# Performance work log

Measured on AMD Instinct MI355X. Metric: run time of the kernel, lower is better.

## Reference

```python
import jax, jax.numpy as jnp
import numpy as np

B = 32768
T = 4096

def setup_inputs() -> dict:
    key = jax.random.key(0)
    k1, k2, k3 = jax.random.split(key, 3)
    q0 = jax.random.normal(k1, (B, 1), dtype=jnp.float32)
    # per-timestep Linear(1,1) weights/biases, flattened to [T]
    w = jax.random.normal(k2, (T,), dtype=jnp.float32)
    b = jax.random.normal(k3, (T,), dtype=jnp.float32)
    return {"q0": q0, "w": w, "b": b}

def reference(q0, w, b):
    # Original: u_seq[b, t, 0] = w[t] * q0[b, 0] + b[t]  (q never updates in the loop)
    # Single fused broadcast replaces T tiny GEMMs.
    u_seq = q0[:, None, :] * w[None, :, None] + b[None, :, None]  # [B, T, 1]
    return u_seq
```

## Files before the change

kernel.cpp:

```cpp
#include <hip/hip_runtime.h>
#include <hip/hip_bf16.h>


__global__ __launch_bounds__(256)
void pn_rowkernel(const float* __restrict__ q0,
                  const float4* __restrict__ w4,
                  const float4* __restrict__ b4,
                  float4* __restrict__ out4,
                  int T4) {
    const int row = blockIdx.x;
    const float q = q0[row];
    float4* __restrict__ orow = out4 + (long long)row * T4;
    for (int j = threadIdx.x; j < T4; j += blockDim.x) {
        const float4 wv = w4[j];
        const float4 bv = b4[j];
        float4 o;
        o.x = fmaf(q, wv.x, bv.x);
        o.y = fmaf(q, wv.y, bv.y);
        o.z = fmaf(q, wv.z, bv.z);
        o.w = fmaf(q, wv.w, bv.w);
        orow[j] = o;
    }
}

__global__ __launch_bounds__(256)
void pn_rowkernel_scalar(const float* __restrict__ q0,
                         const float* __restrict__ w,
                         const float* __restrict__ b,
                         float* __restrict__ out,
                         int T) {
    const int row = blockIdx.x;
    const float q = q0[row];
    float* __restrict__ orow = out + (long long)row * T;
    for (int j = threadIdx.x; j < T; j += blockDim.x) {
        orow[j] = fmaf(q, w[j], b[j]);
    }
}

extern "C" void kernel_launch(void* const* d_in, const int* in_sizes, int n_in,
                              void* d_out, int out_size, void* d_ws, size_t ws_size,
                              hipStream_t stream) {
    const float* q0 = (const float*)d_in[0];
    const float* w  = (const float*)d_in[1];
    const float* b  = (const float*)d_in[2];
    float* out = (float*)d_out;

    const int B = in_sizes[0];
    const int T = in_sizes[1];

    if ((T & 3) == 0) {
        pn_rowkernel<<<B, 256, 0, stream>>>(
            q0,
            reinterpret_cast<const float4*>(w),
            reinterpret_cast<const float4*>(b),
            reinterpret_cast<float4*>(out),
            T >> 2);
    } else {
        pn_rowkernel_scalar<<<B, 256, 0, stream>>>(q0, w, b, out, T);
    }
}
```

Measured before the change: 99.70 us.

## Add column-tiled kernel with register-resident weights and nontemporal stores

Adds a kernel where each thread holds one float4 of w and b in registers and loops over 64 rows. It writes the outputs with nontemporal stores, and the grid is tiled over row groups and column chunks. This removes the repeated w/b loads per row and aims to stream the large output past the caches. The risk is that each block writes strided 4 KB row segments, which may hurt write locality relative to full-row writes.

```diff
diff --git a/kernel.cpp b/kernel.cpp
--- a/kernel.cpp
+++ b/kernel.cpp
@@ -1,6 +1,44 @@
 #include <hip/hip_runtime.h>
 #include <hip/hip_bf16.h>
 
+
+typedef float f32x4 __attribute__((ext_vector_type(4)));
+
+__device__ inline float4 fma4(float q, const float4& w, const float4& b) {
+    float4 o;
+    o.x = fmaf(q, w.x, b.x);
+    o.y = fmaf(q, w.y, b.y);
+    o.z = fmaf(q, w.z, b.z);
+    o.w = fmaf(q, w.w, b.w);
+    return o;
+}
+
+__device__ inline void nt_store4(float4 v, float4* p) {
+    __builtin_nontemporal_store(*reinterpret_cast<f32x4*>(&v),
+                                reinterpret_cast<f32x4*>(p));
+}
+
+__global__ __launch_bounds__(256)
+void pn_colkernel(const float* __restrict__ q0,
+                  const float4* __restrict__ w4,
+                  const float4* __restrict__ b4,
+                  float4* __restrict__ out4,
+                  int T4, int rows_per_blk) {
+    const int t4 = blockIdx.y * blockDim.x + threadIdx.x;
+    const float4 wv = w4[t4];
+    const float4 bv = b4[t4];
+    const int r0 = blockIdx.x * rows_per_blk;
+
+    #pragma unroll 1
+    for (int r = 0; r < rows_per_blk; r += 4) {
+        const float4 qv = *reinterpret_cast<const float4*>(q0 + r0 + r);
+        const long long base = (long long)(r0 + r) * T4 + t4;
+        nt_store4(fma4(qv.x, wv, bv), out4 + base);
+        nt_store4(fma4(qv.y, wv, bv), out4 + base + T4);
+        nt_store4(fma4(qv.z, wv, bv), out4 + base + 2LL * T4);
+        nt_store4(fma4(qv.w, wv, bv), out4 + base + 3LL * T4);
+    }
+}
 
 __global__ __launch_bounds__(256)
 void pn_rowkernel(const float* __restrict__ q0,
@@ -12,14 +50,7 @@
     const float q = q0[row];
     float4* __restrict__ orow = out4 + (long long)row * T4;
     for (int j = threadIdx.x; j < T4; j += blockDim.x) {
-        const float4 wv = w4[j];
-        const float4 bv = b4[j];
-        float4 o;
-        o.x = fmaf(q, wv.x, bv.x);
-        o.y = fmaf(q, wv.y, bv.y);
-        o.z = fmaf(q, wv.z, bv.z);
-        o.w = fmaf(q, wv.w, bv.w);
-        orow[j] = o;
+        orow[j] = fma4(q, w4[j], b4[j]);
     }
 }
 
@@ -48,14 +79,27 @@
     const int B = in_sizes[0];
     const int T = in_sizes[1];
 
-    if ((T & 3) == 0) {
+    if ((T & 3) != 0) {
+        pn_rowkernel_scalar<<<B, 256, 0, stream>>>(q0, w, b, out, T);
+        return;
+    }
+    const int T4 = T >> 2;
+
+    const int rows_per_blk = 64;
+    if ((T4 % 256) == 0 && (B % rows_per_blk) == 0) {
+        dim3 grid(B / rows_per_blk, T4 / 256);
+        pn_colkernel<<<grid, 256, 0, stream>>>(
+            q0,
+            reinterpret_cast<const float4*>(w),
+            reinterpret_cast<const float4*>(b),
+            reinterpret_cast<float4*>(out),
+            T4, rows_per_blk);
+    } else {
         pn_rowkernel<<<B, 256, 0, stream>>>(
             q0,
             reinterpret_cast<const float4*>(w),
             reinterpret_cast<const float4*>(b),
             reinterpret_cast<float4*>(out),
-            T >> 2);
-    } else {
-        pn_rowkernel_scalar<<<B, 256, 0, stream>>>(q0, w, b, out, T);
+            T4);
     }
 }
```

Result: no change. 97.80 us (-1.9%).
